# Kernel optimization log

Hardware: AMD Instinct MI355X
Metric: run time of the kernel (lower is better)

The kernel has to match this reference:

```python
import jax, jax.numpy as jnp
import numpy as np

EMBED = 384
HEADS = 6
HEAD_DIM = EMBED // HEADS
LN_EPS = 1e-5


def setup_inputs() -> dict:
    key = jax.random.key(0)
    ks = jax.random.split(key, 10)
    s = lambda fan_in: 1.0 / np.sqrt(fan_in)
    inp = {
        "x": jax.random.normal(ks[0], (2, 4096, EMBED), dtype=jnp.float32),
        # weights stored as (in, out) so forward is x @ W + b
        "w_qkv": jax.random.uniform(ks[1], (EMBED, 3 * EMBED), minval=-s(EMBED), maxval=s(EMBED)),
        "b_qkv": jnp.zeros((3 * EMBED,), jnp.float32),
        "w_lin": jax.random.uniform(ks[2], (EMBED, EMBED), minval=-s(EMBED), maxval=s(EMBED)),
        "b_lin": jnp.zeros((EMBED,), jnp.float32),
        "g1": jnp.ones((EMBED,), jnp.float32),
        "be1": jnp.zeros((EMBED,), jnp.float32),
        "g2": jnp.ones((EMBED,), jnp.float32),
        "be2": jnp.zeros((EMBED,), jnp.float32),
        "w1": jax.random.uniform(ks[3], (EMBED, 4 * EMBED), minval=-s(EMBED), maxval=s(EMBED)),
        "b1": jnp.zeros((4 * EMBED,), jnp.float32),
        "w2": jax.random.uniform(ks[4], (4 * EMBED, EMBED), minval=-s(4 * EMBED), maxval=s(4 * EMBED)),
        "b2": jnp.zeros((EMBED,), jnp.float32),
    }
    return inp


def _layer_norm(x, g, b):
    mu = jnp.mean(x, axis=-1, keepdims=True)
    var = jnp.mean(jnp.square(x - mu), axis=-1, keepdims=True)
    return (x - mu) * jax.lax.rsqrt(var + LN_EPS) * g + b


def reference(x, w_qkv, b_qkv, w_lin, b_lin, g1, be1, g2, be2, w1, b1, w2, b2):
    B, N, E = x.shape
    # --- MSA block ---
    h = _layer_norm(x, g1, be1)
    qkv = (h @ w_qkv + b_qkv).reshape(B, N, HEADS, 3 * HEAD_DIM)
    q, k, v = jnp.split(qkv, 3, axis=-1)  # each (B, N, H, hd)
    scale = 1.0 / np.sqrt(HEAD_DIM).astype(np.float32)
    scores = jnp.einsum("bihd,bjhd->bijh", q, k) * scale  # (B, N, N, H)
    attn = jax.nn.softmax(scores, axis=2)  # softmax over keys j (dim=-2)
    msa = jnp.einsum("bijh,bjhd->bihd", attn, v).reshape(B, N, E)
    x = msa @ w_lin + b_lin + x
    # --- MLP block ---
    h2 = _layer_norm(x, g2, be2)
    x = jax.nn.gelu(h2 @ w1 + b1, approximate=False) @ w2 + b2 + x
    return x
```

## Files before the change

kernel.cpp:

```cpp
#include <hip/hip_runtime.h>
#include <math.h>

#define EMBED 384
#define HEADS 6
#define HD    64
#define SEQ   4096
#define BATCH 2
#define ROWS  (BATCH * SEQ)
#define QKV_W (3 * EMBED)
#define NSPLIT 3

typedef __bf16 bf16x8 __attribute__((ext_vector_type(8)));
typedef float  f32x16 __attribute__((ext_vector_type(16)));
typedef unsigned short ushort_t;

union U4B { uint4 u; bf16x8 b; };

#define MFMA(a, b, c) __builtin_amdgcn_mfma_f32_32x32x16_bf16(a, b, c, 0, 0, 0)

#define AS1 __attribute__((address_space(1)))
#define AS3 __attribute__((address_space(3)))

__device__ __forceinline__ void gload16(const void* g, void* l) {
    __builtin_amdgcn_global_load_lds((AS1 const unsigned int*)g,
                                     (AS3 unsigned int*)l, 16, 0, 0);
}

__device__ __forceinline__ unsigned short bfbits(float f) {
    return __builtin_bit_cast(unsigned short, (__bf16)f);
}
__device__ __forceinline__ unsigned pack2(float a, float b) {
    return ((unsigned)bfbits(b) << 16) | (unsigned)bfbits(a);
}
__device__ __forceinline__ float max3f(float a, float b, float c) {
    return fmaxf(fmaxf(a, b), c);
}
__device__ __forceinline__ float ex2(float x) {
    return __builtin_amdgcn_exp2f(x);
}

__global__ __launch_bounds__(64) void ln_kernel(const float* __restrict__ x,
                                                const float* __restrict__ g,
                                                const float* __restrict__ b,
                                                ushort_t* __restrict__ out) {
    const int row  = blockIdx.x;
    const int lane = threadIdx.x;
    const float* xr = x + (size_t)row * EMBED;

    float v[6];
    float sum = 0.f;
#pragma unroll
    for (int i = 0; i < 6; ++i) { v[i] = xr[lane + i * 64]; sum += v[i]; }
#pragma unroll
    for (int o = 32; o > 0; o >>= 1) sum += __shfl_xor(sum, o, 64);
    const float mu = sum * (1.f / EMBED);

    float var = 0.f;
#pragma unroll
    for (int i = 0; i < 6; ++i) { const float d = v[i] - mu; var += d * d; }
#pragma unroll
    for (int o = 32; o > 0; o >>= 1) var += __shfl_xor(var, o, 64);
    const float rstd = rsqrtf(var * (1.f / EMBED) + 1e-5f);

    ushort_t* orow = out + (size_t)row * EMBED;
#pragma unroll
    for (int i = 0; i < 6; ++i) {
        const int c = lane + i * 64;
        orow[c] = bfbits((v[i] - mu) * rstd * g[c] + b[c]);
    }
}

__global__ __launch_bounds__(256) void wcvt_all(const float* __restrict__ w_qkv,
                                                const float* __restrict__ w_lin,
                                                const float* __restrict__ w1,
                                                const float* __restrict__ w2,
                                                ushort_t* wqkvT, ushort_t* wlinT,
                                                ushort_t* w1T, ushort_t* w2T) {
    int bid = blockIdx.x;
    const float* W; ushort_t* Wt; int K, N, tx;
    if (bid < 432)       { W = w_qkv; Wt = wqkvT; K = 384;  N = 1152; tx = 36; }
    else if (bid < 576)  { bid -= 432;  W = w_lin; Wt = wlinT; K = 384;  N = 384;  tx = 12; }
    else if (bid < 1152) { bid -= 576;  W = w1;    Wt = w1T;   K = 384;  N = 1536; tx = 48; }
    else                 { bid -= 1152; W = w2;    Wt = w2T;   K = 1536; N = 384;  tx = 12; }
    const int nb = (bid % tx) * 32, kb = (bid / tx) * 32;

    __shared__ float ws[32][33];
    const int tid = threadIdx.x;
    {
        const int r = tid >> 3, c = (tid & 7) * 4;
        const float4 v = *(const float4*)(W + (size_t)(kb + r) * N + nb + c);
        ws[r][c] = v.x; ws[r][c + 1] = v.y; ws[r][c + 2] = v.z; ws[r][c + 3] = v.w;
    }
    __syncthreads();
    const int n = tid >> 3, k0 = (tid & 7) * 4;
    union { ushort_t s[4]; uint2 u; } o;
#pragma unroll
    for (int i = 0; i < 4; ++i) o.s[i] = bfbits(ws[k0 + i][n]);
    *(uint2*)(Wt + (size_t)(nb + n) * K + kb + k0) = o.u;
}

template <int EPI, int BM, int BN>
__global__ __launch_bounds__(256) void gemm_bf16(const ushort_t* __restrict__ A,
                                                 const ushort_t* __restrict__ Bt,
                                                 const float* __restrict__ bias,
                                                 const float* __restrict__ R,
                                                 float* __restrict__ C,
                                                 ushort_t* __restrict__ Hb,
                                                 ushort_t* __restrict__ qbp,
                                                 ushort_t* __restrict__ kbp,
                                                 ushort_t* __restrict__ vrp,
                                                 int N, int K) {
    constexpr int ACH = BM * 8;
    constexpr int BCH = BN * 8;
    constexpr int AR  = BM / 64;
    constexpr int BR  = BN / 64;
    __shared__ uint4 asl[2 * ACH];
    __shared__ uint4 bsl[2 * BCH];

    const int tid = threadIdx.x;
    const int lq = tid & 31, h = (tid >> 5) & 1, w = tid >> 6;
    const int wr = w >> 1, wc = w & 1;
    const int m0 = blockIdx.x * BM, n0 = blockIdx.y * BN;
    const int wbase = tid & 192;

    f32x16 acc[AR][BR];
#pragma unroll
    for (int a = 0; a < AR; ++a)
#pragma unroll
        for (int b = 0; b < BR; ++b)
#pragma unroll
            for (int r = 0; r < 16; ++r) acc[a][b][r] = 0.f;

    auto stage = [&](int s, int buf) {
        const int k0 = s * 64;
#pragma unroll
        for (int u = 0; u < BM / 32; ++u) {
            const int ci = tid + 256 * u;
            const int row = ci >> 3;
            const int chs = (ci & 7) ^ (row & 7);
            gload16((const uint4*)(A + (size_t)(m0 + row) * K + k0) + chs,
                    &asl[buf * ACH + wbase + u * 256]);
        }
#pragma unroll
        for (int u = 0; u < BN / 32; ++u) {
            const int ci = tid + 256 * u;
            const int row = ci >> 3;
            const int chs = (ci & 7) ^ (row & 7);
            gload16((const uint4*)(Bt + (size_t)(n0 + row) * K + k0) + chs,
                    &bsl[buf * BCH + wbase + u * 256]);
        }
    };

    stage(0, 0);
    const int nst = K / 64;
    for (int s = 0; s < nst; ++s) {
        __syncthreads();
        if (s + 1 < nst) stage(s + 1, (s + 1) & 1);
        const int ab = (s & 1) * ACH, bb = (s & 1) * BCH;
#pragma unroll
        for (int ks = 0; ks < 4; ++ks) {
            U4B af[AR], bf[BR];
#pragma unroll
            for (int a = 0; a < AR; ++a) {
                const int rm = wr * (BM / 2) + a * 32 + lq;
                af[a].u = asl[ab + rm * 8 + ((2 * ks + h) ^ (rm & 7))];
            }
#pragma unroll
            for (int b = 0; b < BR; ++b) {
                const int rn = wc * (BN / 2) + b * 32 + lq;
                bf[b].u = bsl[bb + rn * 8 + ((2 * ks + h) ^ (rn & 7))];
            }
            __builtin_amdgcn_s_setprio(1);
#pragma unroll
            for (int a = 0; a < AR; ++a)
#pragma unroll
                for (int b = 0; b < BR; ++b)
                    acc[a][b] = MFMA(af[a].b, bf[b].b, acc[a][b]);
            __builtin_amdgcn_s_setprio(0);
        }
    }

#pragma unroll
    for (int a = 0; a < AR; ++a)
#pragma unroll
        for (int b = 0; b < BR; ++b) {
            const int Cb = n0 + wc * (BN / 2) + b * 32;
            const int c = Cb + lq;
            const float bv = bias[c];
            if (EPI == 0) {
                const int head = Cb / 192, rem = Cb % 192;
                const int role = rem >> 6, d = (rem & 63) + lq;
#pragma unroll
                for (int r = 0; r < 16; ++r) {
                    const int grow = m0 + wr * (BM / 2) + a * 32 + (r & 3) + 8 * (r >> 2) + 4 * h;
                    const int bat = grow >> 12, n = grow & 4095;
                    const size_t idx = ((size_t)(bat * HEADS + head) * SEQ + n) * 64 + d;
                    const float v = acc[a][b][r] + bv;
                    if (role == 0)      qbp[idx] = bfbits(v * 0.1803368801f);
                    else if (role == 1) kbp[idx] = bfbits(v);
                    else                vrp[idx] = bfbits(v);
                }
            } else {
#pragma unroll
                for (int r = 0; r < 16; ++r) {
                    const int row = m0 + wr * (BM / 2) + a * 32 + (r & 3) + 8 * (r >> 2) + 4 * h;
                    const float v = acc[a][b][r] + bv;
                    if (EPI == 1) {
                        C[(size_t)row * N + c] = v + R[(size_t)row * N + c];
                    } else {
                        const float gl = 0.5f * v * (1.f + erff(v * 0.70710678118654752f));
                        Hb[(size_t)row * N + c] = bfbits(gl);
                    }
                }
            }
        }
}

__global__ __launch_bounds__(256) void vtrans(const ushort_t* __restrict__ vr,
                                              ushort_t* __restrict__ vt) {
    __shared__ ushort_t vs[64][72];
    const int nt = blockIdx.x, bh = blockIdx.y;
    const int tid = threadIdx.x;
    const int r = tid >> 2, c0 = (tid & 3) * 16;
    const int n0 = nt * 64;
    {
        const uint4* src = (const uint4*)(vr + ((size_t)bh * SEQ + n0 + r) * 64 + c0);
        union { uint4 u[2]; ushort_t s[16]; } t2;
        t2.u[0] = src[0]; t2.u[1] = src[1];
#pragma unroll
        for (int i = 0; i < 16; ++i) vs[r][c0 + i] = t2.s[i];
    }
    __syncthreads();
#pragma unroll
    for (int u = 0; u < 2; ++u) {
        const int cid = tid * 2 + u;
        const int d = cid >> 3, cc = cid & 7;
        union { ushort_t s[8]; uint4 u4; } ov;
#pragma unroll
        for (int jj = 0; jj < 8; ++jj) ov.s[jj] = vs[cc * 8 + jj][d];
        *(uint4*)(vt + (size_t)bh * 64 * SEQ + (size_t)d * SEQ + n0 + cc * 8) = ov.u4;
    }
}

__global__ __launch_bounds__(256) void attn_kernel(const ushort_t* __restrict__ qb,
                                                   const ushort_t* __restrict__ kb,
                                                   const ushort_t* __restrict__ vt,
                                                   float* __restrict__ opart,
                                                   float* __restrict__ ml) {
    __shared__ uint4 kbl[1024];
    __shared__ uint4 vbl[1024];

    const int tid = threadIdx.x;
    const int lq = tid & 31;
    const int h  = (tid >> 5) & 1;
    const int w  = tid >> 6;
    const int wbase = tid & 192;
    const int bh = blockIdx.y;
    const int z  = blockIdx.z;
    const int q0 = blockIdx.x * 128 + w * 32;

    const ushort_t* kg = kb + (size_t)bh * SEQ * 64;
    const ushort_t* vg = vt + (size_t)bh * 64 * SEQ;

    U4B qf[4];
    {
        const uint4* qrow = (const uint4*)(qb + ((size_t)bh * SEQ + q0 + lq) * 64);
#pragma unroll
        for (int s = 0; s < 4; ++s) qf[s].u = qrow[2 * s + h];
    }

    f32x16 o[2];
#pragma unroll
    for (int dc = 0; dc < 2; ++dc)
#pragma unroll
        for (int r = 0; r < 16; ++r) o[dc][r] = 0.f;
    float m_run = -INFINITY, l_run = 0.f;

    auto stage_tile = [&](int t, int buf) {
#pragma unroll
        for (int u = 0; u < 2; ++u) {
            const int ci = tid + 256 * u;
            const int row = ci >> 3;
            const int chs = (ci & 7) ^ (row & 7);
            gload16((const uint4*)(kg + (size_t)(t * 64 + row) * 64) + chs,
                    &kbl[buf * 512 + wbase + u * 256]);
            gload16((const uint4*)(vg + (size_t)row * SEQ + t * 64) + chs,
                    &vbl[buf * 512 + wbase + u * 256]);
        }
    };

    const int t0 = z * 11;
    const int t1 = min(t0 + 11, SEQ / 128);
    stage_tile(t0, 0);

    for (int t = t0; t < t1; ++t) {
        __syncthreads();
        if (t + 1 < t1) stage_tile(t + 1, (t + 1 - t0) & 1);
        const int bs = ((t - t0) & 1) * 512;

        f32x16 st[2];
#pragma unroll
        for (int kc = 0; kc < 2; ++kc) {
#pragma unroll
            for (int r = 0; r < 16; ++r) st[kc][r] = 0.f;
            __builtin_amdgcn_s_setprio(1);
#pragma unroll
            for (int s = 0; s < 4; ++s) {
                const int row = kc * 32 + lq;
                U4B ka; ka.u = kbl[bs + row * 8 + ((2 * s + h) ^ (row & 7))];
                st[kc] = MFMA(ka.b, qf[s].b, st[kc]);
            }
            __builtin_amdgcn_s_setprio(0);
        }

#define SV(i) st[(i) >> 4][(i) & 15]
        float r3[11];
#pragma unroll
        for (int i = 0; i < 10; ++i) r3[i] = max3f(SV(3 * i), SV(3 * i + 1), SV(3 * i + 2));
        r3[10] = fmaxf(SV(30), SV(31));
        const float s1a = max3f(r3[0], r3[1], r3[2]);
        const float s1b = max3f(r3[3], r3[4], r3[5]);
        const float s1c = max3f(r3[6], r3[7], r3[8]);
        const float s1d = fmaxf(r3[9], r3[10]);
        float pm = fmaxf(max3f(s1a, s1b, s1c), s1d);
#undef SV
        pm = fmaxf(pm, __shfl_xor(pm, 32));

        if (__any(pm - m_run > 8.f)) {
            const float mn = fmaxf(m_run, pm);
            const float f = ex2(m_run - mn);
            l_run *= f;
#pragma unroll
            for (int dc = 0; dc < 2; ++dc)
#pragma unroll
                for (int r = 0; r < 16; ++r) o[dc][r] *= f;
            m_run = mn;
        }

        float rs = 0.f;
#pragma unroll
        for (int kc = 0; kc < 2; ++kc)
#pragma unroll
            for (int r = 0; r < 16; ++r) {
                const float p = ex2(st[kc][r] - m_run);
                st[kc][r] = p;
                rs += p;
            }
        rs += __shfl_xor(rs, 32);
        l_run += rs;

        unsigned pk[2][8];
#pragma unroll
        for (int kc = 0; kc < 2; ++kc)
#pragma unroll
            for (int m = 0; m < 8; ++m)
                pk[kc][m] = pack2(st[kc][2 * m], st[kc][2 * m + 1]);

#pragma unroll
        for (int ks = 0; ks < 4; ++ks) {
            const int kc = ks >> 1;
            const int A0 = 4 * (ks & 1);
            const unsigned c0 = pk[kc][A0 + 0], c1 = pk[kc][A0 + 1];
            const unsigned c2 = pk[kc][A0 + 2], c3 = pk[kc][A0 + 3];
            auto r02 = __builtin_amdgcn_permlane32_swap((int)c0, (int)c2, false, false);
            auto r13 = __builtin_amdgcn_permlane32_swap((int)c1, (int)c3, false, false);
            U4B fb;
            fb.u.x = (unsigned)r02[0];
            fb.u.y = (unsigned)r13[0];
            fb.u.z = (unsigned)r02[1];
            fb.u.w = (unsigned)r13[1];
            __builtin_amdgcn_s_setprio(1);
#pragma unroll
            for (int dc = 0; dc < 2; ++dc) {
                const int row = dc * 32 + lq;
                U4B va; va.u = vbl[bs + row * 8 + ((2 * ks + h) ^ (row & 7))];
                o[dc] = MFMA(va.b, fb.b, o[dc]);
            }
            __builtin_amdgcn_s_setprio(0);
        }
    }

    float* ob = opart + (size_t)(z * (BATCH * HEADS) + bh) * 64 * SEQ;
#pragma unroll
    for (int dc = 0; dc < 2; ++dc)
#pragma unroll
        for (int r = 0; r < 16; ++r) {
            const int d = (r & 3) + 8 * (r >> 2) + 4 * h + 32 * dc;
            ob[(size_t)d * SEQ + q0 + lq] = o[dc][r];
        }
    if (h == 0) {
        float* mlp = ml + (size_t)(z * (BATCH * HEADS) + bh) * 2 * SEQ;
        mlp[q0 + lq] = m_run;
        mlp[SEQ + q0 + lq] = l_run;
    }
}

__global__ __launch_bounds__(256) void attn_combine(const float* __restrict__ opart,
                                                    const float* __restrict__ ml,
                                                    ushort_t* __restrict__ msa) {
    const int bh = blockIdx.y;
    const int q = blockIdx.x * 64 + (threadIdx.x & 63);
    const int w = threadIdx.x >> 6;
    float m[NSPLIT], l[NSPLIT];
#pragma unroll
    for (int z = 0; z < NSPLIT; ++z) {
        const float* mlz = ml + (size_t)(z * (BATCH * HEADS) + bh) * 2 * SEQ;
        m[z] = mlz[q]; l[z] = mlz[SEQ + q];
    }
    const float mm = max3f(m[0], m[1], m[2]);
    float e[NSPLIT], lt = 0.f;
#pragma unroll
    for (int z = 0; z < NSPLIT; ++z) { e[z] = ex2(m[z] - mm); lt += l[z] * e[z]; }
    const float inv = 1.f / lt;
#pragma unroll
    for (int z = 0; z < NSPLIT; ++z) e[z] *= inv;

    union { ushort_t s[16]; uint4 u[2]; } ov;
#pragma unroll
    for (int i = 0; i < 16; ++i) {
        float acc = 0.f;
#pragma unroll
        for (int z = 0; z < NSPLIT; ++z)
            acc += opart[((size_t)(z * (BATCH * HEADS) + bh) * 64 + w * 16 + i) * SEQ + q] * e[z];
        ov.s[i] = bfbits(acc);
    }
    const int b = bh / HEADS, hh = bh % HEADS;
    uint4* dst = (uint4*)(msa + ((size_t)b * SEQ + q) * EMBED + hh * 64 + w * 16);
    dst[0] = ov.u[0]; dst[1] = ov.u[1];
}

extern "C" void kernel_launch(void* const* d_in, const int* in_sizes, int n_in,
                              void* d_out, int out_size, void* d_ws, size_t ws_size,
                              hipStream_t stream) {
    const float* x     = (const float*)d_in[0];
    const float* w_qkv = (const float*)d_in[1];
    const float* b_qkv = (const float*)d_in[2];
    const float* w_lin = (const float*)d_in[3];
    const float* b_lin = (const float*)d_in[4];
    const float* g1    = (const float*)d_in[5];
    const float* be1   = (const float*)d_in[6];
    const float* g2    = (const float*)d_in[7];
    const float* be2   = (const float*)d_in[8];
    const float* w1    = (const float*)d_in[9];
    const float* b1    = (const float*)d_in[10];
    const float* w2    = (const float*)d_in[11];
    const float* b2    = (const float*)d_in[12];
    float* out = (float*)d_out;

    char* wsb = (char*)d_ws;
    ushort_t* h_bf   = (ushort_t*)wsb;  wsb += (size_t)ROWS * EMBED * 2;
    ushort_t* hid_bf = (ushort_t*)wsb;  wsb += (size_t)ROWS * 4 * EMBED * 2;
    float*    x2     = (float*)wsb;     wsb += (size_t)ROWS * EMBED * 4;
    ushort_t* msa_bf = (ushort_t*)wsb;  wsb += (size_t)ROWS * EMBED * 2;
    ushort_t* qbf    = (ushort_t*)wsb;  wsb += (size_t)BATCH * HEADS * SEQ * 64 * 2;
    ushort_t* kbf    = (ushort_t*)wsb;  wsb += (size_t)BATCH * HEADS * SEQ * 64 * 2;
    ushort_t* vraw   = (ushort_t*)wsb;  wsb += (size_t)BATCH * HEADS * SEQ * 64 * 2;
    ushort_t* vt     = (ushort_t*)wsb;  wsb += (size_t)BATCH * HEADS * SEQ * 64 * 2;
    ushort_t* wqkvT  = (ushort_t*)wsb;  wsb += (size_t)QKV_W * EMBED * 2;
    ushort_t* wlinT  = (ushort_t*)wsb;  wsb += (size_t)EMBED * EMBED * 2;
    ushort_t* w1T    = (ushort_t*)wsb;  wsb += (size_t)4 * EMBED * EMBED * 2;
    ushort_t* w2T    = (ushort_t*)wsb;  wsb += (size_t)EMBED * 4 * EMBED * 2;
    float*    mlbuf  = (float*)wsb;     wsb += (size_t)NSPLIT * BATCH * HEADS * 2 * SEQ * 4;
    float* opart = (float*)hid_bf;

    wcvt_all<<<1728, 256, 0, stream>>>(w_qkv, w_lin, w1, w2, wqkvT, wlinT, w1T, w2T);
    ln_kernel<<<ROWS, 64, 0, stream>>>(x, g1, be1, h_bf);
    gemm_bf16<0, 64, 128><<<dim3(ROWS / 64, QKV_W / 128), 256, 0, stream>>>(
        h_bf, wqkvT, b_qkv, nullptr, nullptr, nullptr, qbf, kbf, vraw, QKV_W, EMBED);
    vtrans<<<dim3(SEQ / 64, BATCH * HEADS), 256, 0, stream>>>(vraw, vt);
    attn_kernel<<<dim3(SEQ / 128, BATCH * HEADS, NSPLIT), 256, 0, stream>>>(
        qbf, kbf, vt, opart, mlbuf);
    attn_combine<<<dim3(SEQ / 64, BATCH * HEADS), 256, 0, stream>>>(
        opart, mlbuf, msa_bf);
    gemm_bf16<1, 64, 64><<<dim3(ROWS / 64, EMBED / 64), 256, 0, stream>>>(
        msa_bf, wlinT, b_lin, x, x2, nullptr, nullptr, nullptr, nullptr, EMBED, EMBED);
    ln_kernel<<<ROWS, 64, 0, stream>>>(x2, g2, be2, h_bf);
    gemm_bf16<2, 64, 128><<<dim3(ROWS / 64, 4 * EMBED / 128), 256, 0, stream>>>(
        h_bf, w1T, b1, nullptr, nullptr, hid_bf, nullptr, nullptr, nullptr, 4 * EMBED, EMBED);
    gemm_bf16<1, 64, 64><<<dim3(ROWS / 64, EMBED / 64), 256, 0, stream>>>(
        hid_bf, w2T, b2, x2, out, nullptr, nullptr, nullptr, nullptr, EMBED, 4 * EMBED);
}
```

Measured before the change: 231.0 us.

## Enlarge GEMM tiles, split-K the final GEMM, and pipeline loads with vmcnt waits

```diff
diff --git a/kernel.cpp b/kernel.cpp
--- a/kernel.cpp
+++ b/kernel.cpp
@@ -26,6 +26,12 @@
                                      (AS3 unsigned int*)l, 16, 0, 0);
 }
 
+template <int N>
+__device__ __forceinline__ void vmcnt_wait() {
+    constexpr int enc = (N & 15) | (7 << 4) | (15 << 8) | (((N >> 4) & 3) << 14);
+    __builtin_amdgcn_s_waitcnt(enc);
+}
+
 __device__ __forceinline__ unsigned short bfbits(float f) {
     return __builtin_bit_cast(unsigned short, (__bf16)f);
 }
@@ -39,12 +45,12 @@
     return __builtin_amdgcn_exp2f(x);
 }
 
-__global__ __launch_bounds__(64) void ln_kernel(const float* __restrict__ x,
-                                                const float* __restrict__ g,
-                                                const float* __restrict__ b,
-                                                ushort_t* __restrict__ out) {
-    const int row  = blockIdx.x;
-    const int lane = threadIdx.x;
+__global__ __launch_bounds__(256) void ln_kernel(const float* __restrict__ x,
+                                                 const float* __restrict__ g,
+                                                 const float* __restrict__ b,
+                                                 ushort_t* __restrict__ out) {
+    const int row  = blockIdx.x * 4 + (threadIdx.x >> 6);
+    const int lane = threadIdx.x & 63;
     const float* xr = x + (size_t)row * EMBED;
 
     float v[6];
@@ -109,11 +115,12 @@
                                                  ushort_t* __restrict__ qbp,
                                                  ushort_t* __restrict__ kbp,
                                                  ushort_t* __restrict__ vrp,
-                                                 int N, int K) {
+                                                 int N, int K, int Klen) {
     constexpr int ACH = BM * 8;
     constexpr int BCH = BN * 8;
     constexpr int AR  = BM / 64;
     constexpr int BR  = BN / 64;
+    constexpr int LOADS = (BM + BN) / 32;
     __shared__ uint4 asl[2 * ACH];
     __shared__ uint4 bsl[2 * BCH];
 
@@ -121,6 +128,7 @@
     const int lq = tid & 31, h = (tid >> 5) & 1, w = tid >> 6;
     const int wr = w >> 1, wc = w & 1;
     const int m0 = blockIdx.x * BM, n0 = blockIdx.y * BN;
+    const int kbase = blockIdx.z * Klen;
     const int wbase = tid & 192;
 
     f32x16 acc[AR][BR];
@@ -132,7 +140,7 @@
             for (int r = 0; r < 16; ++r) acc[a][b][r] = 0.f;
 
     auto stage = [&](int s, int buf) {
-        const int k0 = s * 64;
+        const int k0 = kbase + s * 64;
 #pragma unroll
         for (int u = 0; u < BM / 32; ++u) {
             const int ci = tid + 256 * u;
@@ -152,10 +160,17 @@
     };
 
     stage(0, 0);
-    const int nst = K / 64;
+    const int nst = Klen / 64;
     for (int s = 0; s < nst; ++s) {
-        __syncthreads();
-        if (s + 1 < nst) stage(s + 1, (s + 1) & 1);
+        __builtin_amdgcn_s_barrier();
+        if (s + 1 < nst) {
+            stage(s + 1, (s + 1) & 1);
+            vmcnt_wait<LOADS>();
+        } else {
+            vmcnt_wait<0>();
+        }
+        __builtin_amdgcn_s_barrier();
+        __builtin_amdgcn_sched_barrier(0);
         const int ab = (s & 1) * ACH, bb = (s & 1) * BCH;
 #pragma unroll
         for (int ks = 0; ks < 4; ++ks) {
@@ -184,11 +199,11 @@
     for (int a = 0; a < AR; ++a)
 #pragma unroll
         for (int b = 0; b < BR; ++b) {
-            const int Cb = n0 + wc * (BN / 2) + b * 32;
-            const int c = Cb + lq;
+            const int rem = wc * (BN / 2) + b * 32;
+            const int c = n0 + rem + lq;
             const float bv = bias[c];
             if (EPI == 0) {
-                const int head = Cb / 192, rem = Cb % 192;
+                const int head = n0 / 192;
                 const int role = rem >> 6, d = (rem & 63) + lq;
 #pragma unroll
                 for (int r = 0; r < 16; ++r) {
@@ -207,9 +222,13 @@
                     const float v = acc[a][b][r] + bv;
                     if (EPI == 1) {
                         C[(size_t)row * N + c] = v + R[(size_t)row * N + c];
-                    } else {
+                    } else if (EPI == 2) {
                         const float gl = 0.5f * v * (1.f + erff(v * 0.70710678118654752f));
                         Hb[(size_t)row * N + c] = bfbits(gl);
+                    } else {
+                        float pv = acc[a][b][r];
+                        if (blockIdx.z == 0) pv += bv + R[(size_t)row * N + c];
+                        atomicAdd(&C[(size_t)row * N + c], pv);
                     }
                 }
             }
@@ -294,8 +313,15 @@
     stage_tile(t0, 0);
 
     for (int t = t0; t < t1; ++t) {
-        __syncthreads();
-        if (t + 1 < t1) stage_tile(t + 1, (t + 1 - t0) & 1);
+        __builtin_amdgcn_s_barrier();
+        if (t + 1 < t1) {
+            stage_tile(t + 1, (t + 1 - t0) & 1);
+            vmcnt_wait<4>();
+        } else {
+            vmcnt_wait<0>();
+        }
+        __builtin_amdgcn_s_barrier();
+        __builtin_amdgcn_sched_barrier(0);
         const int bs = ((t - t0) & 1) * 512;
 
         f32x16 st[2];
@@ -337,17 +363,22 @@
             m_run = mn;
         }
 
-        float rs = 0.f;
+        float rs0 = 0.f, rs1 = 0.f, rs2 = 0.f, rs3 = 0.f;
 #pragma unroll
         for (int kc = 0; kc < 2; ++kc)
 #pragma unroll
-            for (int r = 0; r < 16; ++r) {
-                const float p = ex2(st[kc][r] - m_run);
-                st[kc][r] = p;
-                rs += p;
+            for (int r = 0; r < 16; r += 4) {
+                const float p0 = ex2(st[kc][r + 0] - m_run);
+                const float p1 = ex2(st[kc][r + 1] - m_run);
+                const float p2 = ex2(st[kc][r + 2] - m_run);
+                const float p3 = ex2(st[kc][r + 3] - m_run);
+                st[kc][r + 0] = p0; st[kc][r + 1] = p1;
+                st[kc][r + 2] = p2; st[kc][r + 3] = p3;
+                rs0 += p0; rs1 += p1; rs2 += p2; rs3 += p3;
             }
-        rs += __shfl_xor(rs, 32);
-        l_run += rs;
+        float rsum = (rs0 + rs1) + (rs2 + rs3);
+        rsum += __shfl_xor(rsum, 32);
+        l_run += rsum;
 
         unsigned pk[2][8];
 #pragma unroll
@@ -464,19 +495,24 @@
     float* opart = (float*)hid_bf;
 
     wcvt_all<<<1728, 256, 0, stream>>>(w_qkv, w_lin, w1, w2, wqkvT, wlinT, w1T, w2T);
-    ln_kernel<<<ROWS, 64, 0, stream>>>(x, g1, be1, h_bf);
-    gemm_bf16<0, 64, 128><<<dim3(ROWS / 64, QKV_W / 128), 256, 0, stream>>>(
-        h_bf, wqkvT, b_qkv, nullptr, nullptr, nullptr, qbf, kbf, vraw, QKV_W, EMBED);
+    ln_kernel<<<ROWS / 4, 256, 0, stream>>>(x, g1, be1, h_bf);
+    gemm_bf16<0, 128, 192><<<dim3(ROWS / 128, QKV_W / 192), 256, 0, stream>>>(
+        h_bf, wqkvT, b_qkv, nullptr, nullptr, nullptr, qbf, kbf, vraw,
+        QKV_W, EMBED, EMBED);
     vtrans<<<dim3(SEQ / 64, BATCH * HEADS), 256, 0, stream>>>(vraw, vt);
     attn_kernel<<<dim3(SEQ / 128, BATCH * HEADS, NSPLIT), 256, 0, stream>>>(
         qbf, kbf, vt, opart, mlbuf);
     attn_combine<<<dim3(SEQ / 64, BATCH * HEADS), 256, 0, stream>>>(
         opart, mlbuf, msa_bf);
-    gemm_bf16<1, 64, 64><<<dim3(ROWS / 64, EMBED / 64), 256, 0, stream>>>(
-        msa_bf, wlinT, b_lin, x, x2, nullptr, nullptr, nullptr, nullptr, EMBED, EMBED);
-    ln_kernel<<<ROWS, 64, 0, stream>>>(x2, g2, be2, h_bf);
-    gemm_bf16<2, 64, 128><<<dim3(ROWS / 64, 4 * EMBED / 128), 256, 0, stream>>>(
-        h_bf, w1T, b1, nullptr, nullptr, hid_bf, nullptr, nullptr, nullptr, 4 * EMBED, EMBED);
-    gemm_bf16<1, 64, 64><<<dim3(ROWS / 64, EMBED / 64), 256, 0, stream>>>(
-        hid_bf, w2T, b2, x2, out, nullptr, nullptr, nullptr, nullptr, EMBED, 4 * EMBED);
-}
+    gemm_bf16<1, 64, 128><<<dim3(ROWS / 64, EMBED / 128), 256, 0, stream>>>(
+        msa_bf, wlinT, b_lin, x, x2, nullptr, nullptr, nullptr, nullptr,
+        EMBED, EMBED, EMBED);
+    ln_kernel<<<ROWS / 4, 256, 0, stream>>>(x2, g2, be2, h_bf);
+    gemm_bf16<2, 128, 192><<<dim3(ROWS / 128, 4 * EMBED / 192), 256, 0, stream>>>(
+        h_bf, w1T, b1, nullptr, nullptr, hid_bf, nullptr, nullptr, nullptr,
+        4 * EMBED, EMBED, EMBED);
+    hipMemsetAsync(d_out, 0, (size_t)out_size * 4, stream);
+    gemm_bf16<3, 128, 192><<<dim3(ROWS / 128, EMBED / 192, 3), 256, 0, stream>>>(
+        hid_bf, w2T, b2, x2, out, nullptr, nullptr, nullptr, nullptr,
+        EMBED, 4 * EMBED, 512);
+}
```

After: 278.1 us. +20.4%, slower.
